# Kernel optimization log

Measured on AMD Instinct MI355X. Metric: run time of the kernel, lower is better.

## Reference

```python
import jax, jax.numpy as jnp
import numpy as np

TEMPERATURE = 0.1
EPS = 1e-8


def setup_inputs() -> dict:
    key = jax.random.key(0)
    k1, k2 = jax.random.split(key)
    features = jax.random.normal(k1, (1024, 256, 16, 8), dtype=jnp.float32)
    labels = jax.random.randint(k2, (1024,), 0, 64, dtype=jnp.int64)
    return {"features": features, "labels": labels}


def reference(features, labels):
    B = features.shape[0]
    f = features.reshape(B, -1)
    norm = jnp.clip(jnp.linalg.norm(f, axis=1, keepdims=True), EPS)
    f = f / norm
    # matcher modeled as cosine-similarity gram matrix (opaque TransMatcher out of scope)
    scores = (f @ f.T) / TEMPERATURE  # [B, B]

    same = labels[:, None] == labels[None, :]
    eye = jnp.eye(B, dtype=bool)
    pos = same & ~eye  # positives excluding self
    neg = ~same & ~eye  # negatives excluding self

    # shared max over pos ∪ neg = all off-diagonal entries per row (matches original)
    row_max = jnp.max(jnp.where(eye, -jnp.inf, scores), axis=1, keepdims=True)
    e = jnp.exp(scores - row_max)  # [B, B]
    pos_sum = jnp.sum(jnp.where(pos, e, 0.0), axis=1)
    neg_sum = jnp.sum(jnp.where(neg, e, 0.0), axis=1)

    valid = jnp.any(pos, axis=1) & jnp.any(neg, axis=1)
    safe_pos = jnp.where(valid, pos_sum, 1.0)
    safe_neg = jnp.where(valid, neg_sum, 1.0)
    # loss_i = neg_term - pos_term; shared max cancels
    loss_i = jnp.where(valid, jnp.log(safe_neg) - jnp.log(safe_pos), 0.0)

    total = jnp.sum(valid.astype(jnp.float32))
    loss = jnp.where(total > 0, jnp.sum(loss_i) / jnp.maximum(total, 1.0), 0.0)

    max_pos = jnp.max(jnp.where(pos, scores, -jnp.inf), axis=1)
    max_neg = jnp.max(jnp.where(neg, scores, -jnp.inf), axis=1)
    correct = jnp.sum((valid & (max_pos > max_neg)).astype(jnp.float32))
    accuracy = jnp.where(total > 0, correct / jnp.maximum(total, 1.0), 0.5)
    return loss, accuracy
```

## Files before the change

kernel.cpp:

```cpp
#include <hip/hip_runtime.h>
#include <hip/hip_bf16.h>
#include <stdint.h>

#define BSZ 1024
#define KF 32768
#define SPLITK 16
#define KPER (KF / SPLITK)
#define BKB 128
#define NKT (KPER / BKB)
#define TEMP_INV 10.0f

typedef float f32x4 __attribute__((ext_vector_type(4)));
typedef int v8i __attribute__((ext_vector_type(8)));

__device__ __forceinline__ void async_copy16(const void* g, void* l) {
    __builtin_amdgcn_global_load_lds(
        (const __attribute__((address_space(1))) void*)g,
        (__attribute__((address_space(3))) void*)l, 16, 0, 0);
}

__device__ __forceinline__ float waveSum(float v) {
    for (int o = 32; o > 0; o >>= 1) v += __shfl_down(v, o);
    return v;
}
__device__ __forceinline__ float waveMax(float v) {
    for (int o = 32; o > 0; o >>= 1) v = fmaxf(v, __shfl_down(v, o));
    return v;
}
__device__ __forceinline__ float blockSum(float v, float* red, int tid) {
    v = waveSum(v);
    __syncthreads();
    if ((tid & 63) == 0) red[tid >> 6] = v;
    __syncthreads();
    return red[0] + red[1] + red[2] + red[3];
}
__device__ __forceinline__ float blockMax(float v, float* red, int tid) {
    v = waveMax(v);
    __syncthreads();
    if ((tid & 63) == 0) red[tid >> 6] = v;
    __syncthreads();
    return fmaxf(fmaxf(red[0], red[1]), fmaxf(red[2], red[3]));
}

__global__ __launch_bounds__(256) void k_norm_convert(
    const float* __restrict__ f, unsigned char* __restrict__ f8,
    float* __restrict__ inv_norm) {
    int row = blockIdx.x, tid = threadIdx.x;
    const float4* src = (const float4*)(f + (size_t)row * KF);
    int4* dst = (int4*)(f8 + (size_t)row * KF);
    float ss = 0.f;
    for (int o = 0; o < 8; ++o) {
        int base4 = o * 1024 + tid * 4;
        int4 pk;
        int* pkp = &pk.x;
#pragma unroll
        for (int q = 0; q < 4; ++q) {
            float4 v = src[base4 + q];
            ss += v.x * v.x + v.y * v.y + v.z * v.z + v.w * v.w;
            int wd = __builtin_amdgcn_cvt_pk_fp8_f32(v.x, v.y, 0, false);
            wd = __builtin_amdgcn_cvt_pk_fp8_f32(v.z, v.w, wd, true);
            pkp[q] = wd;
        }
        dst[o * 256 + tid] = pk;
    }
    __shared__ float red[4];
    float tot = blockSum(ss, red, tid);
    if (tid == 0) inv_norm[row] = 1.0f / fmaxf(sqrtf(tot), 1e-8f);
}

__global__ __launch_bounds__(256) void k_gemm(
    const unsigned char* __restrict__ f8, unsigned char* __restrict__ partials) {
    __shared__ unsigned char Alds[2][128 * BKB];
    __shared__ unsigned char Blds[2][128 * BKB];
    int tid = threadIdx.x;

    int bid = blockIdx.x;
    int g = bid & 7;
    int j = bid >> 3;
    int p = (g << 1) + (j / 36);
    int t = j % 36;

    int bi = 0, accu = 0;
    while (accu + bi + 1 <= t) { accu += bi + 1; ++bi; }
    int bj = t - accu;
    int row0 = bi * 128, col0 = bj * 128;
    size_t kbase = (size_t)p * KPER;

    const unsigned char* Ag = f8 + (size_t)row0 * KF;
    const unsigned char* Bg = f8 + (size_t)col0 * KF;
    int lane = tid & 63, w = tid >> 6;
    int wrow = (w >> 1) * 64, wcol = (w & 1) * 64;
    int mrow = lane & 15, quad = lane >> 4;

    int r_st[4], g_st[4];
#pragma unroll
    for (int c = 0; c < 4; ++c) {
        int idx = c * 256 + tid;
        r_st[c] = idx >> 3;
        g_st[c] = (idx & 7) ^ (r_st[c] & 7);
    }

    f32x4 acc[4][4] = {};

#pragma unroll
    for (int c = 0; c < 4; ++c) {
        int idx = c * 256 + tid;
        async_copy16(Ag + (size_t)r_st[c] * KF + kbase + g_st[c] * 16, &Alds[0][idx * 16]);
        async_copy16(Bg + (size_t)r_st[c] * KF + kbase + g_st[c] * 16, &Blds[0][idx * 16]);
    }
    asm volatile("s_waitcnt vmcnt(0)" ::: "memory");
    __builtin_amdgcn_s_barrier();

#pragma unroll
    for (int kt = 0; kt < NKT; ++kt) {
        int cur = kt & 1;
        if (kt + 1 < NKT) {
            size_t k0 = kbase + (size_t)(kt + 1) * BKB;
#pragma unroll
            for (int c = 0; c < 4; ++c) {
                int idx = c * 256 + tid;
                async_copy16(Ag + (size_t)r_st[c] * KF + k0 + g_st[c] * 16,
                             &Alds[cur ^ 1][idx * 16]);
                async_copy16(Bg + (size_t)r_st[c] * KF + k0 + g_st[c] * 16,
                             &Blds[cur ^ 1][idx * 16]);
            }
        }
        v8i a8[4], b8[4];
#pragma unroll
        for (int mi = 0; mi < 4; ++mi) {
            int rA = wrow + mi * 16 + mrow;
            int4 lo = *(const int4*)&Alds[cur][rA * BKB + ((quad * 2)     ^ (rA & 7)) * 16];
            int4 hi = *(const int4*)&Alds[cur][rA * BKB + ((quad * 2 + 1) ^ (rA & 7)) * 16];
            a8[mi] = (v8i){lo.x, lo.y, lo.z, lo.w, hi.x, hi.y, hi.z, hi.w};
        }
#pragma unroll
        for (int ni = 0; ni < 4; ++ni) {
            int rB = wcol + ni * 16 + mrow;
            int4 lo = *(const int4*)&Blds[cur][rB * BKB + ((quad * 2)     ^ (rB & 7)) * 16];
            int4 hi = *(const int4*)&Blds[cur][rB * BKB + ((quad * 2 + 1) ^ (rB & 7)) * 16];
            b8[ni] = (v8i){lo.x, lo.y, lo.z, lo.w, hi.x, hi.y, hi.z, hi.w};
        }
        __builtin_amdgcn_s_setprio(1);
#pragma unroll
        for (int mi = 0; mi < 4; ++mi)
#pragma unroll
            for (int ni = 0; ni < 4; ++ni)
                acc[mi][ni] = __builtin_amdgcn_mfma_scale_f32_16x16x128_f8f6f4(
                    a8[mi], b8[ni], acc[mi][ni],
                    0, 0,
                    0, 0x7F7F7F7F,
                    0, 0x7F7F7F7F);
        __builtin_amdgcn_s_setprio(0);
        asm volatile("s_waitcnt vmcnt(0) lgkmcnt(0)" ::: "memory");
        __builtin_amdgcn_s_barrier();
    }

    unsigned char* outp = partials + (size_t)p * BSZ * BSZ;
#pragma unroll
    for (int mi = 0; mi < 4; ++mi)
#pragma unroll
        for (int ni = 0; ni < 4; ++ni)
#pragma unroll
            for (int r = 0; r < 4; ++r) {
                int row = row0 + wrow + mi * 16 + quad * 4 + r;
                int col = col0 + wcol + ni * 16 + mrow;
                int b = __builtin_amdgcn_cvt_pk_fp8_f32(
                            acc[mi][ni][r], acc[mi][ni][r], 0, false);
                outp[(size_t)row * BSZ + col] = (unsigned char)(b & 0xFF);
            }
    if (bi != bj) {
#pragma unroll
        for (int mi = 0; mi < 4; ++mi)
#pragma unroll
            for (int ni = 0; ni < 4; ++ni) {
                int rowm = col0 + wcol + ni * 16 + mrow;
                int colm = row0 + wrow + mi * 16 + quad * 4;
                int pk = __builtin_amdgcn_cvt_pk_fp8_f32(
                             acc[mi][ni][0], acc[mi][ni][1], 0, false);
                pk = __builtin_amdgcn_cvt_pk_fp8_f32(
                         acc[mi][ni][2], acc[mi][ni][3], pk, true);
                *(int*)&outp[(size_t)rowm * BSZ + colm] = pk;
            }
    }
}

__global__ __launch_bounds__(256) void k_loss_rows(
    const unsigned char* __restrict__ partials, const float* __restrict__ inv_norm,
    const int* __restrict__ labels, float* __restrict__ rloss,
    float* __restrict__ rvalid, float* __restrict__ rcorr) {
    int i = blockIdx.x, tid = threadIdx.x;
    __shared__ float red[4];
    float inv_i = inv_norm[i];
    int lab_i = labels[i];

    int j4 = tid * 4;
    float sx = 0.f, sy = 0.f, sz = 0.f, sw = 0.f;
#pragma unroll
    for (int p2 = 0; p2 < SPLITK; ++p2) {
        int v = *(const int*)&partials[(size_t)p2 * BSZ * BSZ + (size_t)i * BSZ + j4];
        sx += __builtin_amdgcn_cvt_f32_fp8(v, 0);
        sy += __builtin_amdgcn_cvt_f32_fp8(v, 1);
        sz += __builtin_amdgcn_cvt_f32_fp8(v, 2);
        sw += __builtin_amdgcn_cvt_f32_fp8(v, 3);
    }
    float4 invj = *(const float4*)&inv_norm[j4];
    float s4[4];
    s4[0] = sx * inv_i * invj.x * TEMP_INV;
    s4[1] = sy * inv_i * invj.y * TEMP_INV;
    s4[2] = sz * inv_i * invj.z * TEMP_INV;
    s4[3] = sw * inv_i * invj.w * TEMP_INV;
    int4 labj = *(const int4*)&labels[j4];
    const int* labjp = &labj.x;

    float pos_sum = 0.f, neg_sum = 0.f, mp = -3.0e38f, mn = -3.0e38f;
#pragma unroll
    for (int q = 0; q < 4; ++q) {
        int j = j4 + q;
        if (j == i) continue;
        float s = s4[q];
        float e = __expf(s - 10.0f);
        if (labjp[q] == lab_i) { pos_sum += e; mp = fmaxf(mp, s); }
        else                   { neg_sum += e; mn = fmaxf(mn, s); }
    }
    float ps = blockSum(pos_sum, red, tid);
    float ns = blockSum(neg_sum, red, tid);
    float mpa = blockMax(mp, red, tid);
    float mna = blockMax(mn, red, tid);
    if (tid == 0) {
        bool valid = (mpa > -1.0e37f) && (mna > -1.0e37f);
        rloss[i]  = valid ? (logf(ns) - logf(ps)) : 0.f;
        rvalid[i] = valid ? 1.f : 0.f;
        rcorr[i]  = (valid && (mpa > mna)) ? 1.f : 0.f;
    }
}

__global__ __launch_bounds__(256) void k_final(
    const float* __restrict__ rloss, const float* __restrict__ rvalid,
    const float* __restrict__ rcorr, float* __restrict__ out) {
    __shared__ float red[4];
    int tid = threadIdx.x;
    float sl = 0.f, sv = 0.f, sc = 0.f;
    for (int c = 0; c < 4; ++c) {
        int j = c * 256 + tid;
        sl += rloss[j]; sv += rvalid[j]; sc += rcorr[j];
    }
    sl = blockSum(sl, red, tid);
    sv = blockSum(sv, red, tid);
    sc = blockSum(sc, red, tid);
    if (tid == 0) {
        out[0] = (sv > 0.f) ? sl / fmaxf(sv, 1.f) : 0.f;
        out[1] = (sv > 0.f) ? sc / fmaxf(sv, 1.f) : 0.5f;
    }
}

extern "C" void kernel_launch(void* const* d_in, const int* in_sizes, int n_in,
                              void* d_out, int out_size, void* d_ws, size_t ws_size,
                              hipStream_t stream) {
    const float* feats = (const float*)d_in[0];
    const int* labels = (const int*)d_in[1];
    float* out = (float*)d_out;
    char* ws = (char*)d_ws;

    unsigned char* f8       = (unsigned char*)ws;
    unsigned char* partials = (unsigned char*)(ws + (size_t)32 * 1024 * 1024);
    float* inv_norm         = (float*)(ws + (size_t)64 * 1024 * 1024);
    float* rloss            = inv_norm + BSZ;
    float* rvalid           = rloss + BSZ;
    float* rcorr            = rvalid + BSZ;

    k_norm_convert<<<BSZ, 256, 0, stream>>>(feats, f8, inv_norm);
    k_gemm<<<dim3(36 * SPLITK), 256, 0, stream>>>(f8, partials);
    k_loss_rows<<<BSZ, 256, 0, stream>>>(partials, inv_norm, labels, rloss, rvalid, rcorr);
    k_final<<<1, 256, 0, stream>>>(rloss, rvalid, rcorr, out);
}
```

Baseline: 236.4 us.

## Load B operand directly from global into registers, drop B LDS staging

The B tile is no longer staged through LDS. Each wave loads its own B fragments straight from global memory into registers, double-buffered one K-step ahead, and launch bounds now ask for two blocks per SM. This halves LDS use and removes the B shared-memory reads, aiming for higher occupancy and less LDS traffic. In exchange, B data is no longer shared through LDS, so the two waves covering the same columns each fetch it from global/L2, and the prefetch registers raise register pressure.

```diff
diff --git a/kernel.cpp b/kernel.cpp
--- a/kernel.cpp
+++ b/kernel.cpp
@@ -68,10 +68,9 @@
     if (tid == 0) inv_norm[row] = 1.0f / fmaxf(sqrtf(tot), 1e-8f);
 }
 
-__global__ __launch_bounds__(256) void k_gemm(
+__global__ __launch_bounds__(256, 2) void k_gemm(
     const unsigned char* __restrict__ f8, unsigned char* __restrict__ partials) {
     __shared__ unsigned char Alds[2][128 * BKB];
-    __shared__ unsigned char Blds[2][128 * BKB];
     int tid = threadIdx.x;
 
     int bid = blockIdx.x;
@@ -100,13 +99,24 @@
         g_st[c] = (idx & 7) ^ (r_st[c] & 7);
     }
 
+    const unsigned char* bq[4];
+#pragma unroll
+    for (int ni = 0; ni < 4; ++ni)
+        bq[ni] = Bg + (size_t)(wcol + ni * 16 + mrow) * KF + quad * 32;
+
     f32x4 acc[4][4] = {};
+    v8i b_pf[2][4];
 
 #pragma unroll
     for (int c = 0; c < 4; ++c) {
         int idx = c * 256 + tid;
         async_copy16(Ag + (size_t)r_st[c] * KF + kbase + g_st[c] * 16, &Alds[0][idx * 16]);
-        async_copy16(Bg + (size_t)r_st[c] * KF + kbase + g_st[c] * 16, &Blds[0][idx * 16]);
+    }
+#pragma unroll
+    for (int ni = 0; ni < 4; ++ni) {
+        int4 lo = *(const int4*)(bq[ni] + kbase);
+        int4 hi = *(const int4*)(bq[ni] + kbase + 16);
+        b_pf[0][ni] = (v8i){lo.x, lo.y, lo.z, lo.w, hi.x, hi.y, hi.z, hi.w};
     }
     asm volatile("s_waitcnt vmcnt(0)" ::: "memory");
     __builtin_amdgcn_s_barrier();
@@ -115,17 +125,22 @@
     for (int kt = 0; kt < NKT; ++kt) {
         int cur = kt & 1;
         if (kt + 1 < NKT) {
-            size_t k0 = kbase + (size_t)(kt + 1) * BKB;
+            size_t k0n = kbase + (size_t)(kt + 1) * BKB;
 #pragma unroll
             for (int c = 0; c < 4; ++c) {
                 int idx = c * 256 + tid;
-                async_copy16(Ag + (size_t)r_st[c] * KF + k0 + g_st[c] * 16,
+                async_copy16(Ag + (size_t)r_st[c] * KF + k0n + g_st[c] * 16,
                              &Alds[cur ^ 1][idx * 16]);
-                async_copy16(Bg + (size_t)r_st[c] * KF + k0 + g_st[c] * 16,
-                             &Blds[cur ^ 1][idx * 16]);
+            }
+#pragma unroll
+            for (int ni = 0; ni < 4; ++ni) {
+                int4 lo = *(const int4*)(bq[ni] + k0n);
+                int4 hi = *(const int4*)(bq[ni] + k0n + 16);
+                b_pf[(kt + 1) & 1][ni] = (v8i){lo.x, lo.y, lo.z, lo.w,
+                                               hi.x, hi.y, hi.z, hi.w};
             }
         }
-        v8i a8[4], b8[4];
+        v8i a8[4];
 #pragma unroll
         for (int mi = 0; mi < 4; ++mi) {
             int rA = wrow + mi * 16 + mrow;
@@ -133,20 +148,13 @@
             int4 hi = *(const int4*)&Alds[cur][rA * BKB + ((quad * 2 + 1) ^ (rA & 7)) * 16];
             a8[mi] = (v8i){lo.x, lo.y, lo.z, lo.w, hi.x, hi.y, hi.z, hi.w};
         }
-#pragma unroll
-        for (int ni = 0; ni < 4; ++ni) {
-            int rB = wcol + ni * 16 + mrow;
-            int4 lo = *(const int4*)&Blds[cur][rB * BKB + ((quad * 2)     ^ (rB & 7)) * 16];
-            int4 hi = *(const int4*)&Blds[cur][rB * BKB + ((quad * 2 + 1) ^ (rB & 7)) * 16];
-            b8[ni] = (v8i){lo.x, lo.y, lo.z, lo.w, hi.x, hi.y, hi.z, hi.w};
-        }
         __builtin_amdgcn_s_setprio(1);
 #pragma unroll
         for (int mi = 0; mi < 4; ++mi)
 #pragma unroll
             for (int ni = 0; ni < 4; ++ni)
                 acc[mi][ni] = __builtin_amdgcn_mfma_scale_f32_16x16x128_f8f6f4(
-                    a8[mi], b8[ni], acc[mi][ni],
+                    a8[mi], b_pf[cur][ni], acc[mi][ni],
                     0, 0,
                     0, 0x7F7F7F7F,
                     0, 0x7F7F7F7F);
```

Measured after the change: 264.8 us. 1.12x slower.

## Single-buffer B tile via register staging, reuse A tile on diagonal blocks

Applied to the files above, without the earlier changes.

Shrinks LDS use in the split-K FP8 GEMM by single-buffering the B tile, staging its next k-slice in registers and storing it to LDS at the top of each iteration. Diagonal tiles skip loading B and read the A tile instead. Launch bounds request 3 blocks per SM, so the smaller LDS footprint can buy more resident blocks. In exchange it adds an extra barrier per k-step, and the register-staged B loads are exposed to global latency instead of going through async direct-to-LDS copies.

```diff
diff --git a/kernel.cpp b/kernel.cpp
--- a/kernel.cpp
+++ b/kernel.cpp
@@ -68,10 +68,10 @@
     if (tid == 0) inv_norm[row] = 1.0f / fmaxf(sqrtf(tot), 1e-8f);
 }
 
-__global__ __launch_bounds__(256) void k_gemm(
+__global__ __launch_bounds__(256, 3) void k_gemm(
     const unsigned char* __restrict__ f8, unsigned char* __restrict__ partials) {
     __shared__ unsigned char Alds[2][128 * BKB];
-    __shared__ unsigned char Blds[2][128 * BKB];
+    __shared__ unsigned char Blds[128 * BKB];
     int tid = threadIdx.x;
 
     int bid = blockIdx.x;
@@ -83,6 +83,7 @@
     int bi = 0, accu = 0;
     while (accu + bi + 1 <= t) { accu += bi + 1; ++bi; }
     int bj = t - accu;
+    bool diag = (bi == bj);
     int row0 = bi * 128, col0 = bj * 128;
     size_t kbase = (size_t)p * KPER;
 
@@ -101,12 +102,17 @@
     }
 
     f32x4 acc[4][4] = {};
+    int4 breg[4];
 
 #pragma unroll
     for (int c = 0; c < 4; ++c) {
         int idx = c * 256 + tid;
         async_copy16(Ag + (size_t)r_st[c] * KF + kbase + g_st[c] * 16, &Alds[0][idx * 16]);
-        async_copy16(Bg + (size_t)r_st[c] * KF + kbase + g_st[c] * 16, &Blds[0][idx * 16]);
+    }
+    if (!diag) {
+#pragma unroll
+        for (int c = 0; c < 4; ++c)
+            breg[c] = *(const int4*)(Bg + (size_t)r_st[c] * KF + kbase + g_st[c] * 16);
     }
     asm volatile("s_waitcnt vmcnt(0)" ::: "memory");
     __builtin_amdgcn_s_barrier();
@@ -114,6 +120,11 @@
 #pragma unroll
     for (int kt = 0; kt < NKT; ++kt) {
         int cur = kt & 1;
+        if (!diag) {
+#pragma unroll
+            for (int c = 0; c < 4; ++c)
+                *(int4*)&Blds[(c * 256 + tid) * 16] = breg[c];
+        }
         if (kt + 1 < NKT) {
             size_t k0 = kbase + (size_t)(kt + 1) * BKB;
 #pragma unroll
@@ -121,11 +132,14 @@
                 int idx = c * 256 + tid;
                 async_copy16(Ag + (size_t)r_st[c] * KF + k0 + g_st[c] * 16,
                              &Alds[cur ^ 1][idx * 16]);
-                async_copy16(Bg + (size_t)r_st[c] * KF + k0 + g_st[c] * 16,
-                             &Blds[cur ^ 1][idx * 16]);
-            }
-        }
-        v8i a8[4], b8[4];
+            }
+            if (!diag) {
+#pragma unroll
+                for (int c = 0; c < 4; ++c)
+                    breg[c] = *(const int4*)(Bg + (size_t)r_st[c] * KF + k0 + g_st[c] * 16);
+            }
+        }
+        v8i a8[4];
 #pragma unroll
         for (int mi = 0; mi < 4; ++mi) {
             int rA = wrow + mi * 16 + mrow;
@@ -133,11 +147,15 @@
             int4 hi = *(const int4*)&Alds[cur][rA * BKB + ((quad * 2 + 1) ^ (rA & 7)) * 16];
             a8[mi] = (v8i){lo.x, lo.y, lo.z, lo.w, hi.x, hi.y, hi.z, hi.w};
         }
+        asm volatile("s_waitcnt lgkmcnt(0)" ::: "memory");
+        __builtin_amdgcn_s_barrier();
+        const unsigned char* Bl = diag ? &Alds[cur][0] : &Blds[0];
+        v8i b8[4];
 #pragma unroll
         for (int ni = 0; ni < 4; ++ni) {
             int rB = wcol + ni * 16 + mrow;
-            int4 lo = *(const int4*)&Blds[cur][rB * BKB + ((quad * 2)     ^ (rB & 7)) * 16];
-            int4 hi = *(const int4*)&Blds[cur][rB * BKB + ((quad * 2 + 1) ^ (rB & 7)) * 16];
+            int4 lo = *(const int4*)&Bl[rB * BKB + ((quad * 2)     ^ (rB & 7)) * 16];
+            int4 hi = *(const int4*)&Bl[rB * BKB + ((quad * 2 + 1) ^ (rB & 7)) * 16];
             b8[ni] = (v8i){lo.x, lo.y, lo.z, lo.w, hi.x, hi.y, hi.z, hi.w};
         }
         __builtin_amdgcn_s_setprio(1);
@@ -168,7 +186,7 @@
                             acc[mi][ni][r], acc[mi][ni][r], 0, false);
                 outp[(size_t)row * BSZ + col] = (unsigned char)(b & 0xFF);
             }
-    if (bi != bj) {
+    if (!diag) {
 #pragma unroll
         for (int mi = 0; mi < 4; ++mi)
 #pragma unroll
@@ -215,8 +233,8 @@
     float pos_sum = 0.f, neg_sum = 0.f, mp = -3.0e38f, mn = -3.0e38f;
 #pragma unroll
     for (int q = 0; q < 4; ++q) {
-        int j = j4 + q;
-        if (j == i) continue;
+        int jj = j4 + q;
+        if (jj == i) continue;
         float s = s4[q];
         float e = __expf(s - 10.0f);
         if (labjp[q] == lab_i) { pos_sum += e; mp = fmaxf(mp, s); }
```

Result: slower. 500.2 us (+111.5%).
